# Performance work log

Hardware: AMD Instinct MI355X
Metric: run time of the kernel (lower is better)

The kernel has to match this reference:

```python
import jax, jax.numpy as jnp
import numpy as np

ALPHA = 0.2   # LeakyReLU negative slope
NEG = -9e15   # mask fill value from the torch code


def _conv1d(x, w, b):
    # x: (N, C_in, L), w: (C_out, C_in, 5), padding=2 -> same length
    y = jax.lax.conv_general_dilated(x, w, window_strides=(1,), padding=[(2, 2)],
                                     dimension_numbers=('NCH', 'OIH', 'NCH'))
    return y + b[None, :, None]


def _gat(h, mask, W, a):
    # Faithful to a_input @ a: e_ij = leakyrelu(Wh_i . a[:H] + Wh_j . a[H:])
    Wh = jnp.einsum('bnf,fo->bno', h, W)          # (B,N,H)
    H = W.shape[1]
    f1 = Wh @ a[:H]                               # (B,N,1)
    f2 = Wh @ a[H:]                               # (B,N,1)
    e = f1 + jnp.swapaxes(f2, 1, 2)               # (B,N,N)
    e = jnp.where(e > 0, e, ALPHA * e)            # LeakyReLU
    e = jnp.where(mask, e, NEG)
    att = jax.nn.softmax(e, axis=-1)              # dropout skipped (eval mode)
    return jnp.einsum('bij,bjo->bio', att, Wh)


def setup_inputs() -> dict:
    key = jax.random.key(0)
    ks = jax.random.split(key, 14)
    B, S, N, H, E = 8, 200, 512, 64, 2048
    sc = 0.1
    return {
        'x': jax.random.normal(ks[0], (B, S, N * 2), dtype=jnp.float32),
        'adj': jax.random.randint(ks[1], (N, N), 0, 2, dtype=jnp.int32),
        'edge_index': jax.random.randint(ks[2], (E, 2), 0, N, dtype=jnp.int32),
        'conv1_w': jax.random.normal(ks[3], (H // 2, 2, 5), dtype=jnp.float32) * sc,
        'conv1_b': jnp.zeros((H // 2,), dtype=jnp.float32),
        'conv2_w': jax.random.normal(ks[4], (H, H // 2, 5), dtype=jnp.float32) * sc,
        'conv2_b': jnp.zeros((H,), dtype=jnp.float32),
        'W1': jax.random.normal(ks[5], (H, H), dtype=jnp.float32) * sc,
        'a1': jax.random.normal(ks[6], (2 * H, 1), dtype=jnp.float32) * sc,
        'W2': jax.random.normal(ks[7], (H, H), dtype=jnp.float32) * sc,
        'a2': jax.random.normal(ks[8], (2 * H, 1), dtype=jnp.float32) * sc,
        'fc1_w': jax.random.normal(ks[9], (2 * H, H), dtype=jnp.float32) * sc,
        'fc1_b': jnp.zeros((H,), dtype=jnp.float32),
        'fc2_w': jax.random.normal(ks[10], (H, 1), dtype=jnp.float32) * sc,
        'fc2_b': jnp.zeros((1,), dtype=jnp.float32),
    }


def reference(x, adj, edge_index, conv1_w, conv1_b, conv2_w, conv2_b,
              W1, a1, W2, a2, fc1_w, fc1_b, fc2_w, fc2_b):
    B = x.shape[0]
    N = adj.shape[0]
    # (B,S,2N) -> (B,N,S,2) -> (B*N,2,S)
    xn = x.reshape(B, -1, N, 2).transpose(0, 2, 1, 3)
    xf = xn.reshape(B * N, -1, 2).transpose(0, 2, 1)
    h = jax.nn.relu(_conv1d(xf, conv1_w, conv1_b))
    h = jax.nn.relu(_conv1d(h, conv2_w, conv2_b))
    h = h.mean(axis=-1)                 # AdaptiveAvgPool1d(1) + squeeze
    h = h.reshape(B, N, -1)             # (B,N,H)
    mask = (adj > 0)[None]              # (1,N,N) broadcasts over batch
    h = jax.nn.relu(_gat(h, mask, W1, a1))
    h = _gat(h, mask, W2, a2)
    h1 = h[:, edge_index[:, 0]]         # (B,E,H)
    h2 = h[:, edge_index[:, 1]]
    he = jnp.concatenate([h1, h2], axis=-1)  # (B,E,2H)
    z = jax.nn.relu(he @ fc1_w + fc1_b)
    return jax.nn.sigmoid(z @ fc2_w + fc2_b).squeeze(-1)  # (B,E)
```

## Files before the change

kernel.cpp:

```cpp
#include <hip/hip_runtime.h>
#include <hip/hip_bf16.h>

typedef unsigned short u16;
typedef __attribute__((ext_vector_type(8))) short short8;
typedef __attribute__((ext_vector_type(4))) float float4v;

#define BATCH 8
#define SLEN  200
#define NNODE 512
#define NEDGE 2048
#define NEGV  -9000000000000000.0f

#define H1S 40
#define H1R 212

__device__ __forceinline__ u16 f2bf(float f) {
    unsigned int x = __float_as_uint(f);
    unsigned int lsb = (x >> 16) & 1u;
    x += 0x7fffu + lsb;
    return (u16)(x >> 16);
}

__device__ __forceinline__ float bf2f(u16 u) {
    return __uint_as_float(((unsigned int)u) << 16);
}

__device__ __forceinline__ unsigned int pk2(float a, float b) {
    __hip_bfloat162 h = __float22bfloat162_rn(make_float2(a, b));
    unsigned int r;
    __builtin_memcpy(&r, &h, 4);
    return r;
}

__global__ __launch_bounds__(256) void pre_kernel(
    const float* __restrict__ x,
    const float* __restrict__ w2,
    const float* __restrict__ fc1w,
    float* __restrict__ xT,
    u16* __restrict__ w2f,
    u16* __restrict__ efw)
{
    __shared__ float tile[32][33];
    const int t = threadIdx.x;
    const int blk = blockIdx.x;

    if (blk < 1792) {
        const int xi  = blk & 31;
        const int rem = blk >> 5;
        const int yi  = rem % 7;
        const int zi  = rem / 7;
        const int nc0 = xi * 32;
        const int s0  = yi * 32;
        const int c   = t & 31, rr = t >> 5;
        #pragma unroll
        for (int r = 0; r < 4; ++r) {
            const int s = s0 + rr + r * 8;
            if (s < SLEN)
                tile[rr + r * 8][c] = x[((size_t)(zi * SLEN + s)) * 1024 + nc0 + c];
        }
        __syncthreads();
        #pragma unroll
        for (int r = 0; r < 4; ++r) {
            const int nc = nc0 + rr + r * 8;
            const int s = s0 + c;
            if (s < SLEN)
                xT[((size_t)(zi * 1024 + nc)) * SLEN + s] = tile[c][rr + r * 8];
        }
        return;
    }

    const int lane = t & 63, wv = t >> 6;
    const int ml = lane & 15, q = lane >> 4;

    for (int fid = wv; fid < 20; fid += 4) {
        const int kk = fid >> 2, ot = fid & 3;
        const int oc = ot * 16 + ml;
        #pragma unroll
        for (int j = 0; j < 8; ++j) {
            const int c  = q * 8 + j;
            const int ic = (c & 1) * 16 + (c >> 1);
            w2f[(fid * 64 + lane) * 8 + j] = f2bf(w2[(size_t)oc * 160 + ic * 5 + kk]);
        }
    }
    for (int u = wv; u < 16; u += 4) {
        const int ks = u >> 2, wvv = u & 3;
        const int o = wvv * 16 + ml;
        #pragma unroll
        for (int j = 0; j < 8; ++j) {
            const int k = ks * 32 + q * 8 + j;
            efw[(u * 64 + lane) * 8 + j] = f2bf(fc1w[k * 64 + o]);
        }
    }
}

__global__ __launch_bounds__(256) void conv_fused_kernel(
    const float* __restrict__ xT,
    const float* __restrict__ w1,
    const float* __restrict__ b1,
    const float* __restrict__ b2,
    const float* __restrict__ W1,
    const float* __restrict__ a1,
    const u16* __restrict__ w2f,
    u16* __restrict__ Wh_bt,
    float* __restrict__ f1,
    float* __restrict__ f2)
{
    __shared__ float xs[2][212];
    __shared__ __align__(16) u16 h1p[H1R * H1S];
    __shared__ float red[4][32];
    __shared__ float hm[64];
    __shared__ float part[4][64];

    const int t    = threadIdx.x;
    const int blk  = blockIdx.x;
    const int b    = blk >> 9;
    const int n    = blk & 511;
    const int lane = t & 63;
    const int wv   = t >> 6;
    const int ml   = lane & 15;
    const int q    = lane >> 4;

    const int p = t & 15;
    const int g = t >> 4;

    const int o2 = wv & 1;
    const int mh = wv >> 1;

    short8 wfA[5], wfB[5];
    #pragma unroll
    for (int kk = 0; kk < 5; ++kk) {
        wfA[kk] = *(const short8*)(w2f + ((kk * 4 + o2 * 2 + 0) * 64 + lane) * 8);
        wfB[kk] = *(const short8*)(w2f + ((kk * 4 + o2 * 2 + 1) * 64 + lane) * 8);
    }
    const float bias2a = b2[o2 * 32 + ml];
    const float bias2b = b2[o2 * 32 + 16 + ml];

    float wA[10], wB[10];
    #pragma unroll
    for (int j = 0; j < 10; ++j) {
        wA[j] = w1[p * 10 + j];
        wB[j] = w1[(16 + p) * 10 + j];
    }
    const float b1a = b1[p], b1b = b1[16 + p];

    if (t < SLEN) {
        const float* xp = xT + ((size_t)(b * 1024 + 2 * n)) * SLEN + t;
        xs[0][2 + t] = xp[0];
        xs[1][2 + t] = xp[SLEN];
    } else if (t < 212) {
        const int pp = (t < 202) ? (t - 200) : t;
        xs[0][pp] = 0.f;
        xs[1][pp] = 0.f;
    }
    {
        unsigned int* hz = (unsigned int*)h1p;
        if (t < 40)       hz[t] = 0u;
        else if (t < 240) hz[4000 + t] = 0u;
    }
    __syncthreads();

    #pragma unroll
    for (int u = 0; u < 4; ++u) {
        const int base = 4 * g + 64 * u;
        if (base < SLEN) {
            float X0[8], X1[8];
            *(float4*)&X0[0] = *(const float4*)&xs[0][base];
            *(float4*)&X0[4] = *(const float4*)&xs[0][base + 4];
            *(float4*)&X1[0] = *(const float4*)&xs[1][base];
            *(float4*)&X1[4] = *(const float4*)&xs[1][base + 4];
            #pragma unroll
            for (int i = 0; i < 4; ++i) {
                float a0 = b1a, a1 = b1b;
                #pragma unroll
                for (int k = 0; k < 5; ++k) {
                    const float x0 = X0[i + k], x1 = X1[i + k];
                    a0 += wA[k] * x0 + wA[5 + k] * x1;
                    a1 += wB[k] * x0 + wB[5 + k] * x1;
                }
                *(unsigned int*)&h1p[(2 + base + i) * H1S + 2 * p] =
                    pk2(fmaxf(a0, 0.f), fmaxf(a1, 0.f));
            }
        }
    }
    __syncthreads();

    float tA = 0.f, tB = 0.f;
    const int mt0 = mh * 7, mtE = mh ? 13 : 7;
    for (int mt = mt0; mt < mtE; ++mt) {
        float4v acc0 = {0.f, 0.f, 0.f, 0.f};
        float4v acc1 = {0.f, 0.f, 0.f, 0.f};
        #pragma unroll
        for (int kk = 0; kk < 5; ++kk) {
            const short8 a = *(const short8*)&h1p[(mt * 16 + ml + kk) * H1S + q * 8];
            acc0 = __builtin_amdgcn_mfma_f32_16x16x32_bf16(a, wfA[kk], acc0, 0, 0, 0);
            acc1 = __builtin_amdgcn_mfma_f32_16x16x32_bf16(a, wfB[kk], acc1, 0, 0, 0);
        }
        if (mt < 12) {
            #pragma unroll
            for (int r = 0; r < 4; ++r) {
                tA += fmaxf(acc0[r] + bias2a, 0.f);
                tB += fmaxf(acc1[r] + bias2b, 0.f);
            }
        } else if (q < 2) {
            #pragma unroll
            for (int r = 0; r < 4; ++r) {
                tA += fmaxf(acc0[r] + bias2a, 0.f);
                tB += fmaxf(acc1[r] + bias2b, 0.f);
            }
        }
    }
    tA += __shfl_xor(tA, 16, 64);
    tA += __shfl_xor(tA, 32, 64);
    tB += __shfl_xor(tB, 16, 64);
    tB += __shfl_xor(tB, 32, 64);
    if (lane < 16) {
        red[wv][ml]      = tA;
        red[wv][16 + ml] = tB;
    }
    __syncthreads();
    if (t < 64) {
        const int grp = t >> 5, idx = t & 31;
        hm[t] = (red[grp][idx] + red[grp + 2][idx]) * (1.0f / 200.0f);
    }
    __syncthreads();

    {
        const int o = t & 63, q4 = t >> 6;
        const float* Wp = W1 + (q4 * 16) * 64 + o;
        float pv = 0.f;
        #pragma unroll
        for (int k = 0; k < 16; ++k) pv += hm[q4 * 16 + k] * Wp[k * 64];
        part[q4][o] = pv;
    }
    __syncthreads();
    if (t < 64) {
        const float v = part[0][t] + part[1][t] + part[2][t] + part[3][t];
        Wh_bt[((size_t)(b * 64 + t)) * 512 + n] = f2bf(v);
        float v1 = v * a1[t];
        float v2 = v * a1[64 + t];
        #pragma unroll
        for (int off = 32; off; off >>= 1) {
            v1 += __shfl_xor(v1, off, 64);
            v2 += __shfl_xor(v2, off, 64);
        }
        if (t == 0) { f1[b * 512 + n] = v1; f2[b * 512 + n] = v2; }
    }
}

__global__ __launch_bounds__(256) void gat_wh_kernel(
    const float* __restrict__ h,
    const float* __restrict__ W,
    const float* __restrict__ a,
    u16* __restrict__ Wh_bt,
    float* __restrict__ f1,
    float* __restrict__ f2)
{
    __shared__ __align__(16) u16 hA[64 * 72];
    __shared__ __align__(16) u16 Wt[64 * 72];
    __shared__ __align__(16) u16 whT[64 * 72];
    __shared__ float as[128];

    const int t    = threadIdx.x;
    const int blk  = blockIdx.x;
    const int b    = blk >> 3;
    const int j0   = (blk & 7) * 64;
    const int lane = t & 63, wv = t >> 6, ml = lane & 15, q = lane >> 4;

    {
        const int r = t >> 2, c0 = (t & 3) * 16;
        const float* hp = h + ((size_t)(b * 512 + j0 + r)) * 64 + c0;
        #pragma unroll
        for (int v = 0; v < 4; ++v) {
            float4 f = *(const float4*)(hp + v * 4);
            unsigned int* dst = (unsigned int*)&hA[r * 72 + c0 + v * 4];
            dst[0] = pk2(f.x, f.y);
            dst[1] = pk2(f.z, f.w);
        }
    }
    {
        const int k = t >> 2, o0 = (t & 3) * 16;
        const float* wp = W + k * 64 + o0;
        #pragma unroll
        for (int v = 0; v < 16; ++v)
            Wt[(o0 + v) * 72 + k] = f2bf(wp[v]);
    }
    if (t < 128) as[t] = a[t];
    __syncthreads();

    short8 af0 = *(const short8*)&hA[(16 * wv + ml) * 72 + q * 8];
    short8 af1 = *(const short8*)&hA[(16 * wv + ml) * 72 + 32 + q * 8];
    float4v acc[4];
    #pragma unroll
    for (int nt = 0; nt < 4; ++nt) {
        short8 b0 = *(const short8*)&Wt[(16 * nt + ml) * 72 + q * 8];
        short8 b1 = *(const short8*)&Wt[(16 * nt + ml) * 72 + 32 + q * 8];
        float4v c = {0.f, 0.f, 0.f, 0.f};
        c = __builtin_amdgcn_mfma_f32_16x16x32_bf16(af0, b0, c, 0, 0, 0);
        c = __builtin_amdgcn_mfma_f32_16x16x32_bf16(af1, b1, c, 0, 0, 0);
        acc[nt] = c;
    }

    #pragma unroll
    for (int nt = 0; nt < 4; ++nt) {
        unsigned int* dst = (unsigned int*)&whT[(16 * nt + ml) * 72 + 16 * wv + q * 4];
        dst[0] = pk2(acc[nt][0], acc[nt][1]);
        dst[1] = pk2(acc[nt][2], acc[nt][3]);
    }

    #pragma unroll
    for (int r = 0; r < 4; ++r) {
        float v1 = 0.f, v2 = 0.f;
        #pragma unroll
        for (int nt = 0; nt < 4; ++nt) {
            const float w = acc[nt][r];
            v1 += w * as[16 * nt + ml];
            v2 += w * as[64 + 16 * nt + ml];
        }
        v1 += __shfl_xor(v1, 1, 64); v2 += __shfl_xor(v2, 1, 64);
        v1 += __shfl_xor(v1, 2, 64); v2 += __shfl_xor(v2, 2, 64);
        v1 += __shfl_xor(v1, 4, 64); v2 += __shfl_xor(v2, 4, 64);
        v1 += __shfl_xor(v1, 8, 64); v2 += __shfl_xor(v2, 8, 64);
        if (ml == 0) {
            const int j = j0 + 16 * wv + q * 4 + r;
            f1[b * 512 + j] = v1;
            f2[b * 512 + j] = v2;
        }
    }
    __syncthreads();

    {
        const int o = t >> 2, js = (t & 3) * 16;
        u16* dst = Wh_bt + ((size_t)(b * 64 + o)) * 512 + j0 + js;
        *(short8*)dst = *(const short8*)&whT[o * 72 + js];
    }
}

#define PSTR 520
__global__ __launch_bounds__(512) void gat_attn_kernel(
    const u16* __restrict__ Wh_bt,
    const float* __restrict__ f1,
    const float* __restrict__ f2,
    const int* __restrict__ adj,
    float* __restrict__ outp,
    const int do_relu)
{
    __shared__ __align__(16) u16 P[16 * PSTR];
    __shared__ float f2s[512];
    __shared__ float invs[16];
    __shared__ float f1s[16];
    __shared__ float accH[4][64][4];

    const int t   = threadIdx.x;
    const int blk = blockIdx.x;
    const int b   = blk >> 5;
    const int i0  = (blk & 31) * 16;

    f2s[t & 511] = f2[b * 512 + (t & 511)];
    if (t < 16) f1s[t] = f1[b * 512 + i0 + t];
    __syncthreads();

    {
        const int i = t >> 5, jseg = t & 31;
        const float f1i = f1s[i];
        const int* arow = adj + (size_t)(i0 + i) * 512 + jseg * 16;
        const float* f2p = f2s + jseg * 16;
        float ev[16];
        float mx = -3.0e38f;
        #pragma unroll
        for (int v = 0; v < 4; ++v) {
            const int4 a4 = *(const int4*)(arow + v * 4);
            #pragma unroll
            for (int u = 0; u < 4; ++u) {
                const int msk = (&a4.x)[u];
                float e = f1i + f2p[v * 4 + u];
                e = e > 0.f ? e : 0.2f * e;
                e = (msk > 0) ? e : NEGV;
                ev[v * 4 + u] = e;
                mx = fmaxf(mx, e);
            }
        }
        mx = fmaxf(mx, __shfl_xor(mx, 1, 64));
        mx = fmaxf(mx, __shfl_xor(mx, 2, 64));
        mx = fmaxf(mx, __shfl_xor(mx, 4, 64));
        mx = fmaxf(mx, __shfl_xor(mx, 8, 64));
        mx = fmaxf(mx, __shfl_xor(mx, 16, 64));
        float sum = 0.f;
        #pragma unroll
        for (int v = 0; v < 16; ++v) {
            const float ex = __expf(ev[v] - mx);
            ev[v] = ex;
            sum += ex;
        }
        sum += __shfl_xor(sum, 1, 64);
        sum += __shfl_xor(sum, 2, 64);
        sum += __shfl_xor(sum, 4, 64);
        sum += __shfl_xor(sum, 8, 64);
        sum += __shfl_xor(sum, 16, 64);
        if (jseg == 0) invs[i] = 1.0f / sum;
        unsigned int* prow = (unsigned int*)&P[i * PSTR + jseg * 16];
        #pragma unroll
        for (int v = 0; v < 8; ++v)
            prow[v] = pk2(ev[2 * v], ev[2 * v + 1]);
    }
    __syncthreads();

    const int lane = t & 63, wv = t >> 6, nt = wv & 3, kh = wv >> 2;
    const int ml = lane & 15, q = lane >> 4;
    const u16* Bp = Wh_bt + ((size_t)(b * 64 + nt * 16 + ml)) * 512 + kh * 256 + q * 8;
    float4v acc = {0.f, 0.f, 0.f, 0.f};
    #pragma unroll
    for (int ks = 0; ks < 8; ++ks) {
        const short8 afr = *(const short8*)&P[ml * PSTR + kh * 256 + ks * 32 + q * 8];
        const short8 bfr = *(const short8*)(Bp + ks * 32);
        acc = __builtin_amdgcn_mfma_f32_16x16x32_bf16(afr, bfr, acc, 0, 0, 0);
    }
    if (kh == 1) {
        #pragma unroll
        for (int r = 0; r < 4; ++r) accH[nt][lane][r] = acc[r];
    }
    __syncthreads();
    if (kh == 0) {
        #pragma unroll
        for (int r = 0; r < 4; ++r) {
            const int i2 = q * 4 + r;
            float val = (acc[r] + accH[nt][lane][r]) * invs[i2];
            if (do_relu) val = fmaxf(val, 0.f);
            outp[((size_t)(b * 512 + i0 + i2)) * 64 + nt * 16 + ml] = val;
        }
    }
}

#define FSTR 136
__global__ __launch_bounds__(256) void edge_mlp_kernel(
    const float* __restrict__ hg,
    const int* __restrict__ eidx,
    const u16* __restrict__ efw,
    const float* __restrict__ fc1b,
    const float* __restrict__ fc2w,
    const float* __restrict__ fc2b,
    float* __restrict__ out)
{
    __shared__ __align__(16) u16 he[16 * FSTR];
    __shared__ float part[16][4];

    const int t   = threadIdx.x;
    const int blk = blockIdx.x;
    const int b   = blk >> 7;
    const int e0  = (blk & 127) * 16;
    const int lane = t & 63, wv = t >> 6, ml = lane & 15, q = lane >> 4;

    short8 bw[4];
    #pragma unroll
    for (int ks = 0; ks < 4; ++ks)
        bw[ks] = *(const short8*)(efw + ((ks * 4 + wv) * 64 + lane) * 8);
    const int o = 16 * wv + ml;
    const float bo = fc1b[o];
    const float wo = fc2w[o];

    {
        const int ep = t >> 4, p = t & 15;
        const int e = e0 + ep;
        const int node = (p < 8) ? eidx[e * 2] : eidx[e * 2 + 1];
        const int c0 = (p & 7) * 8;
        const float* hp = hg + ((size_t)(b * 512 + node)) * 64 + c0;
        const float4 fa = *(const float4*)hp;
        const float4 fb = *(const float4*)(hp + 4);
        unsigned int* dst = (unsigned int*)&he[ep * FSTR + ((p < 8) ? 0 : 64) + c0];
        dst[0] = pk2(fa.x, fa.y);
        dst[1] = pk2(fa.z, fa.w);
        dst[2] = pk2(fb.x, fb.y);
        dst[3] = pk2(fb.z, fb.w);
    }
    __syncthreads();

    float4v acc = {0.f, 0.f, 0.f, 0.f};
    #pragma unroll
    for (int ks = 0; ks < 4; ++ks) {
        const short8 afr = *(const short8*)&he[ml * FSTR + ks * 32 + q * 8];
        acc = __builtin_amdgcn_mfma_f32_16x16x32_bf16(afr, bw[ks], acc, 0, 0, 0);
    }
    #pragma unroll
    for (int r = 0; r < 4; ++r) {
        float z = fmaxf(acc[r] + bo, 0.f) * wo;
        z += __shfl_xor(z, 1, 64);
        z += __shfl_xor(z, 2, 64);
        z += __shfl_xor(z, 4, 64);
        z += __shfl_xor(z, 8, 64);
        if (ml == 0) part[q * 4 + r][wv] = z;
    }
    __syncthreads();
    if (t < 16) {
        const float v = part[t][0] + part[t][1] + part[t][2] + part[t][3] + fc2b[0];
        out[b * 2048 + e0 + t] = 1.0f / (1.0f + __expf(-v));
    }
}

extern "C" void kernel_launch(void* const* d_in, const int* in_sizes, int n_in,
                              void* d_out, int out_size, void* d_ws, size_t ws_size,
                              hipStream_t stream) {
    const float* x    = (const float*)d_in[0];
    const int* adj    = (const int*)d_in[1];
    const int* eidx   = (const int*)d_in[2];
    const float* w1   = (const float*)d_in[3];
    const float* b1   = (const float*)d_in[4];
    const float* w2   = (const float*)d_in[5];
    const float* b2   = (const float*)d_in[6];
    const float* W1   = (const float*)d_in[7];
    const float* a1   = (const float*)d_in[8];
    const float* W2   = (const float*)d_in[9];
    const float* a2   = (const float*)d_in[10];
    const float* fc1w = (const float*)d_in[11];
    const float* fc1b = (const float*)d_in[12];
    const float* fc2w = (const float*)d_in[13];
    const float* fc2b = (const float*)d_in[14];
    float* out = (float*)d_out;

    float* ws = (float*)d_ws;
    const size_t R = (size_t)BATCH * NNODE;
    float* g    = ws;
    float* f1   = g + R * 64;
    float* f2   = f1 + R;
    u16*   whbt = (u16*)(f2 + R);
    u16*   w2f  = whbt + R * 64;
    u16*   efw  = w2f + 10240;
    float* xT   = (float*)(efw + 8192);

    pre_kernel<<<dim3(1793), dim3(256), 0, stream>>>(x, w2, fc1w, xT, w2f, efw);
    conv_fused_kernel<<<dim3(4096), dim3(256), 0, stream>>>(
        xT, w1, b1, b2, W1, a1, w2f, whbt, f1, f2);
    gat_attn_kernel<<<dim3(256), dim3(512), 0, stream>>>(whbt, f1, f2, adj, g, 1);
    gat_wh_kernel<<<dim3(64), dim3(256), 0, stream>>>(g, W2, a2, whbt, f1, f2);
    gat_attn_kernel<<<dim3(256), dim3(512), 0, stream>>>(whbt, f1, f2, adj, g, 0);
    edge_mlp_kernel<<<dim3(1024), dim3(256), 0, stream>>>(
        g, eidx, efw, fc1b, fc2w, fc2b, out);
}
```

Before: 142.5 us.

## Fuse second GAT projection into first attention kernel and bit-pack adjacency mask

The separate gat_wh kernel is removed. The first attention kernel now computes relu(att@Wh), multiplies it by a pre-converted bf16 W2 with MFMA, and writes the second layer's Wh (transposed) and the f1/f2 logits directly. That saves one launch and the float round trip of the intermediate through global memory. The adjacency matrix is also packed once into 64-bit ballot masks in pre_kernel, so both attention passes read 32 KB of bits instead of 1 MB of ints. The cost is extra syncs and shared memory in the attention kernel, and double-buffered f1/f2/Wh workspace.

```diff
diff --git a/kernel.cpp b/kernel.cpp
--- a/kernel.cpp
+++ b/kernel.cpp
@@ -2,6 +2,7 @@
 #include <hip/hip_bf16.h>
 
 typedef unsigned short u16;
+typedef unsigned long long u64;
 typedef __attribute__((ext_vector_type(8))) short short8;
 typedef __attribute__((ext_vector_type(4))) float float4v;
 
@@ -34,15 +35,20 @@
 
 __global__ __launch_bounds__(256) void pre_kernel(
     const float* __restrict__ x,
+    const int* __restrict__ adj,
     const float* __restrict__ w2,
     const float* __restrict__ fc1w,
+    const float* __restrict__ W2g,
     float* __restrict__ xT,
     u16* __restrict__ w2f,
-    u16* __restrict__ efw)
+    u16* __restrict__ efw,
+    u16* __restrict__ w2gf,
+    u64* __restrict__ msk)
 {
     __shared__ float tile[32][33];
     const int t = threadIdx.x;
     const int blk = blockIdx.x;
+    const int lane = t & 63, wv = t >> 6;
 
     if (blk < 1792) {
         const int xi  = blk & 31;
@@ -69,7 +75,19 @@
         return;
     }
 
-    const int lane = t & 63, wv = t >> 6;
+    if (blk < 1800) {
+        const int r0 = (blk - 1792) * 64;
+        for (int i = r0 + wv; i < r0 + 64; i += 4) {
+            #pragma unroll
+            for (int c = 0; c < 8; ++c) {
+                const int v = adj[(size_t)i * 512 + c * 64 + lane];
+                const u64 m = __ballot(v > 0);
+                if (lane == 0) msk[i * 8 + c] = m;
+            }
+        }
+        return;
+    }
+
     const int ml = lane & 15, q = lane >> 4;
 
     for (int fid = wv; fid < 20; fid += 4) {
@@ -89,6 +107,15 @@
         for (int j = 0; j < 8; ++j) {
             const int k = ks * 32 + q * 8 + j;
             efw[(u * 64 + lane) * 8 + j] = f2bf(fc1w[k * 64 + o]);
+        }
+    }
+    for (int u = wv; u < 8; u += 4) {
+        const int kh = u >> 2, nt = u & 3;
+        const int o = nt * 16 + ml;
+        #pragma unroll
+        for (int j = 0; j < 8; ++j) {
+            const int k = kh * 32 + q * 8 + j;
+            w2gf[(u * 64 + lane) * 8 + j] = f2bf(W2g[k * 64 + o]);
         }
     }
 }
@@ -119,10 +146,8 @@
     const int wv   = t >> 6;
     const int ml   = lane & 15;
     const int q    = lane >> 4;
-
     const int p = t & 15;
     const int g = t >> 4;
-
     const int o2 = wv & 1;
     const int mh = wv >> 1;
 
@@ -170,15 +195,15 @@
             *(float4*)&X1[4] = *(const float4*)&xs[1][base + 4];
             #pragma unroll
             for (int i = 0; i < 4; ++i) {
-                float a0 = b1a, a1 = b1b;
+                float a0 = b1a, a1v = b1b;
                 #pragma unroll
                 for (int k = 0; k < 5; ++k) {
                     const float x0 = X0[i + k], x1 = X1[i + k];
-                    a0 += wA[k] * x0 + wA[5 + k] * x1;
-                    a1 += wB[k] * x0 + wB[5 + k] * x1;
+                    a0  += wA[k] * x0 + wA[5 + k] * x1;
+                    a1v += wB[k] * x0 + wB[5 + k] * x1;
                 }
                 *(unsigned int*)&h1p[(2 + base + i) * H1S + 2 * p] =
-                    pk2(fmaxf(a0, 0.f), fmaxf(a1, 0.f));
+                    pk2(fmaxf(a0, 0.f), fmaxf(a1v, 0.f));
             }
         }
     }
@@ -247,137 +272,53 @@
     }
 }
 
-__global__ __launch_bounds__(256) void gat_wh_kernel(
-    const float* __restrict__ h,
-    const float* __restrict__ W,
-    const float* __restrict__ a,
-    u16* __restrict__ Wh_bt,
-    float* __restrict__ f1,
-    float* __restrict__ f2)
-{
-    __shared__ __align__(16) u16 hA[64 * 72];
-    __shared__ __align__(16) u16 Wt[64 * 72];
-    __shared__ __align__(16) u16 whT[64 * 72];
-    __shared__ float as[128];
-
-    const int t    = threadIdx.x;
-    const int blk  = blockIdx.x;
-    const int b    = blk >> 3;
-    const int j0   = (blk & 7) * 64;
-    const int lane = t & 63, wv = t >> 6, ml = lane & 15, q = lane >> 4;
-
-    {
-        const int r = t >> 2, c0 = (t & 3) * 16;
-        const float* hp = h + ((size_t)(b * 512 + j0 + r)) * 64 + c0;
-        #pragma unroll
-        for (int v = 0; v < 4; ++v) {
-            float4 f = *(const float4*)(hp + v * 4);
-            unsigned int* dst = (unsigned int*)&hA[r * 72 + c0 + v * 4];
-            dst[0] = pk2(f.x, f.y);
-            dst[1] = pk2(f.z, f.w);
-        }
-    }
-    {
-        const int k = t >> 2, o0 = (t & 3) * 16;
-        const float* wp = W + k * 64 + o0;
-        #pragma unroll
-        for (int v = 0; v < 16; ++v)
-            Wt[(o0 + v) * 72 + k] = f2bf(wp[v]);
-    }
-    if (t < 128) as[t] = a[t];
-    __syncthreads();
-
-    short8 af0 = *(const short8*)&hA[(16 * wv + ml) * 72 + q * 8];
-    short8 af1 = *(const short8*)&hA[(16 * wv + ml) * 72 + 32 + q * 8];
-    float4v acc[4];
-    #pragma unroll
-    for (int nt = 0; nt < 4; ++nt) {
-        short8 b0 = *(const short8*)&Wt[(16 * nt + ml) * 72 + q * 8];
-        short8 b1 = *(const short8*)&Wt[(16 * nt + ml) * 72 + 32 + q * 8];
-        float4v c = {0.f, 0.f, 0.f, 0.f};
-        c = __builtin_amdgcn_mfma_f32_16x16x32_bf16(af0, b0, c, 0, 0, 0);
-        c = __builtin_amdgcn_mfma_f32_16x16x32_bf16(af1, b1, c, 0, 0, 0);
-        acc[nt] = c;
-    }
-
-    #pragma unroll
-    for (int nt = 0; nt < 4; ++nt) {
-        unsigned int* dst = (unsigned int*)&whT[(16 * nt + ml) * 72 + 16 * wv + q * 4];
-        dst[0] = pk2(acc[nt][0], acc[nt][1]);
-        dst[1] = pk2(acc[nt][2], acc[nt][3]);
-    }
-
-    #pragma unroll
-    for (int r = 0; r < 4; ++r) {
-        float v1 = 0.f, v2 = 0.f;
-        #pragma unroll
-        for (int nt = 0; nt < 4; ++nt) {
-            const float w = acc[nt][r];
-            v1 += w * as[16 * nt + ml];
-            v2 += w * as[64 + 16 * nt + ml];
-        }
-        v1 += __shfl_xor(v1, 1, 64); v2 += __shfl_xor(v2, 1, 64);
-        v1 += __shfl_xor(v1, 2, 64); v2 += __shfl_xor(v2, 2, 64);
-        v1 += __shfl_xor(v1, 4, 64); v2 += __shfl_xor(v2, 4, 64);
-        v1 += __shfl_xor(v1, 8, 64); v2 += __shfl_xor(v2, 8, 64);
-        if (ml == 0) {
-            const int j = j0 + 16 * wv + q * 4 + r;
-            f1[b * 512 + j] = v1;
-            f2[b * 512 + j] = v2;
-        }
-    }
-    __syncthreads();
-
-    {
-        const int o = t >> 2, js = (t & 3) * 16;
-        u16* dst = Wh_bt + ((size_t)(b * 64 + o)) * 512 + j0 + js;
-        *(short8*)dst = *(const short8*)&whT[o * 72 + js];
-    }
-}
-
 #define PSTR 520
 __global__ __launch_bounds__(512) void gat_attn_kernel(
     const u16* __restrict__ Wh_bt,
-    const float* __restrict__ f1,
-    const float* __restrict__ f2,
-    const int* __restrict__ adj,
+    const float* __restrict__ f1in,
+    const float* __restrict__ f2in,
+    const u64* __restrict__ msk,
+    const u16* __restrict__ w2gf,
+    const float* __restrict__ a2,
+    u16* __restrict__ whbt_out,
+    float* __restrict__ f1out,
+    float* __restrict__ f2out,
     float* __restrict__ outp,
-    const int do_relu)
+    const int fuse)
 {
     __shared__ __align__(16) u16 P[16 * PSTR];
     __shared__ float f2s[512];
     __shared__ float invs[16];
     __shared__ float f1s[16];
     __shared__ float accH[4][64][4];
+    __shared__ __align__(16) u16 g1s[16 * 72];
+    __shared__ __align__(16) u16 wh2s[64 * 20];
+    __shared__ float fp1[4][16], fp2[4][16];
 
     const int t   = threadIdx.x;
     const int blk = blockIdx.x;
     const int b   = blk >> 5;
     const int i0  = (blk & 31) * 16;
 
-    f2s[t & 511] = f2[b * 512 + (t & 511)];
-    if (t < 16) f1s[t] = f1[b * 512 + i0 + t];
+    f2s[t & 511] = f2in[b * 512 + (t & 511)];
+    if (t < 16) f1s[t] = f1in[b * 512 + i0 + t];
     __syncthreads();
 
     {
         const int i = t >> 5, jseg = t & 31;
         const float f1i = f1s[i];
-        const int* arow = adj + (size_t)(i0 + i) * 512 + jseg * 16;
+        const unsigned int mbits =
+            ((const u16*)msk)[(size_t)(i0 + i) * 32 + jseg];
         const float* f2p = f2s + jseg * 16;
         float ev[16];
         float mx = -3.0e38f;
         #pragma unroll
-        for (int v = 0; v < 4; ++v) {
-            const int4 a4 = *(const int4*)(arow + v * 4);
-            #pragma unroll
-            for (int u = 0; u < 4; ++u) {
-                const int msk = (&a4.x)[u];
-                float e = f1i + f2p[v * 4 + u];
-                e = e > 0.f ? e : 0.2f * e;
-                e = (msk > 0) ? e : NEGV;
-                ev[v * 4 + u] = e;
-                mx = fmaxf(mx, e);
-            }
+        for (int v = 0; v < 16; ++v) {
+            float e = f1i + f2p[v];
+            e = e > 0.f ? e : 0.2f * e;
+            e = ((mbits >> v) & 1u) ? e : NEGV;
+            ev[v] = e;
+            mx = fmaxf(mx, e);
         }
         mx = fmaxf(mx, __shfl_xor(mx, 1, 64));
         mx = fmaxf(mx, __shfl_xor(mx, 2, 64));
@@ -424,9 +365,54 @@
         for (int r = 0; r < 4; ++r) {
             const int i2 = q * 4 + r;
             float val = (acc[r] + accH[nt][lane][r]) * invs[i2];
-            if (do_relu) val = fmaxf(val, 0.f);
-            outp[((size_t)(b * 512 + i0 + i2)) * 64 + nt * 16 + ml] = val;
-        }
+            if (fuse) {
+                val = fmaxf(val, 0.f);
+                g1s[i2 * 72 + nt * 16 + ml] = f2bf(val);
+            } else {
+                outp[((size_t)(b * 512 + i0 + i2)) * 64 + nt * 16 + ml] = val;
+            }
+        }
+    }
+
+    if (!fuse) return;
+
+    __syncthreads();
+    const short8 af2 = *(const short8*)&g1s[ml * 72 + kh * 32 + q * 8];
+    const short8 bf2v = *(const short8*)(w2gf + ((kh * 4 + nt) * 64 + lane) * 8);
+    float4v c2 = {0.f, 0.f, 0.f, 0.f};
+    c2 = __builtin_amdgcn_mfma_f32_16x16x32_bf16(af2, bf2v, c2, 0, 0, 0);
+    if (kh == 1) {
+        #pragma unroll
+        for (int r = 0; r < 4; ++r) accH[nt][lane][r] = c2[r];
+    }
+    __syncthreads();
+    if (kh == 0) {
+        const int o = nt * 16 + ml;
+        const float a2o1 = a2[o], a2o2 = a2[64 + o];
+        #pragma unroll
+        for (int r = 0; r < 4; ++r) {
+            const float wv2 = c2[r] + accH[nt][lane][r];
+            wh2s[o * 20 + q * 4 + r] = f2bf(wv2);
+            float p1 = wv2 * a2o1, p2 = wv2 * a2o2;
+            p1 += __shfl_xor(p1, 1, 64); p2 += __shfl_xor(p2, 1, 64);
+            p1 += __shfl_xor(p1, 2, 64); p2 += __shfl_xor(p2, 2, 64);
+            p1 += __shfl_xor(p1, 4, 64); p2 += __shfl_xor(p2, 4, 64);
+            p1 += __shfl_xor(p1, 8, 64); p2 += __shfl_xor(p2, 8, 64);
+            if (ml == 0) {
+                fp1[nt][q * 4 + r] = p1;
+                fp2[nt][q * 4 + r] = p2;
+            }
+        }
+    }
+    __syncthreads();
+    if (t < 256) {
+        const int o = t >> 2, seg = t & 3;
+        *(uint2*)&whbt_out[((size_t)(b * 64 + o)) * 512 + i0 + seg * 4] =
+            *(const uint2*)&wh2s[o * 20 + seg * 4];
+    }
+    if (t < 16) {
+        f1out[b * 512 + i0 + t] = fp1[0][t] + fp1[1][t] + fp1[2][t] + fp1[3][t];
+        f2out[b * 512 + i0 + t] = fp2[0][t] + fp2[1][t] + fp2[2][t] + fp2[3][t];
     }
 }
 
@@ -517,20 +503,27 @@
 
     float* ws = (float*)d_ws;
     const size_t R = (size_t)BATCH * NNODE;
-    float* g    = ws;
-    float* f1   = g + R * 64;
-    float* f2   = f1 + R;
-    u16*   whbt = (u16*)(f2 + R);
-    u16*   w2f  = whbt + R * 64;
-    u16*   efw  = w2f + 10240;
-    float* xT   = (float*)(efw + 8192);
-
-    pre_kernel<<<dim3(1793), dim3(256), 0, stream>>>(x, w2, fc1w, xT, w2f, efw);
+    float* g     = ws;
+    float* f1a   = g + R * 64;
+    float* f2a   = f1a + R;
+    float* f1b   = f2a + R;
+    float* f2b   = f1b + R;
+    u16*   whbt1 = (u16*)(f2b + R);
+    u16*   whbt2 = whbt1 + R * 64;
+    u16*   w2f   = whbt2 + R * 64;
+    u16*   efw   = w2f + 10240;
+    u16*   w2gf  = efw + 8192;
+    u64*   msk   = (u64*)(w2gf + 4096);
+    float* xT    = (float*)(msk + 4096);
+
+    pre_kernel<<<dim3(1801), dim3(256), 0, stream>>>(
+        x, adj, w2, fc1w, W2, xT, w2f, efw, w2gf, msk);
     conv_fused_kernel<<<dim3(4096), dim3(256), 0, stream>>>(
-        xT, w1, b1, b2, W1, a1, w2f, whbt, f1, f2);
-    gat_attn_kernel<<<dim3(256), dim3(512), 0, stream>>>(whbt, f1, f2, adj, g, 1);
-    gat_wh_kernel<<<dim3(64), dim3(256), 0, stream>>>(g, W2, a2, whbt, f1, f2);
-    gat_attn_kernel<<<dim3(256), dim3(512), 0, stream>>>(whbt, f1, f2, adj, g, 0);
+        xT, w1, b1, b2, W1, a1, w2f, whbt1, f1a, f2a);
+    gat_attn_kernel<<<dim3(256), dim3(512), 0, stream>>>(
+        whbt1, f1a, f2a, msk, w2gf, a2, whbt2, f1b, f2b, g, 1);
+    gat_attn_kernel<<<dim3(256), dim3(512), 0, stream>>>(
+        whbt2, f1b, f2b, msk, w2gf, a2, whbt2, f1b, f2b, g, 0);
     edge_mlp_kernel<<<dim3(1024), dim3(256), 0, stream>>>(
         g, eidx, efw, fc1b, fc2w, fc2b, out);
 }
```

New measurement: 167.9 us. 1.18x slower.
